# Kernel optimization log

Measured on AMD Instinct MI355X. Metric: run time of the kernel, lower is better.

Reference implementation:

```python
import jax, jax.numpy as jnp
import numpy as np

N_NODES = 50000
N_EDGES = 800000
D_IN = 128
D_HID = 128
BN_EPS = 1e-5


def _sage_mean(h, src, dst, w_self, w_neigh, b):
    # DGL SAGEConv('mean'): out = h @ W_self + mean_{neighbors}(h_src) @ W_neigh + bias
    msg = h[src]                                               # [E, D] gather
    ssum = jax.ops.segment_sum(msg, dst, num_segments=N_NODES)  # [N, D]
    deg = jax.ops.segment_sum(jnp.ones((src.shape[0],), h.dtype), dst,
                              num_segments=N_NODES)            # [N]
    mean = ssum / jnp.maximum(deg, 1.0)[:, None]
    return h @ w_self + mean @ w_neigh + b


def _bn_relu(h, gamma, beta):
    # BatchNorm1d with batch statistics (training-mode math), then ReLU.
    m = jnp.mean(h, axis=0)
    v = jnp.mean(jnp.square(h - m), axis=0)  # biased variance, as torch uses for normalization
    hn = (h - m) * jax.lax.rsqrt(v + BN_EPS) * gamma + beta
    return jax.nn.relu(hn)


def setup_inputs() -> dict:
    key = jax.random.key(0)
    ks = jax.random.split(key, 16)
    x = jax.random.normal(ks[0], (N_NODES, D_IN), dtype=jnp.float32)
    src = jax.random.randint(ks[1], (N_EDGES,), 0, N_NODES, dtype=jnp.int32)
    dst = jax.random.randint(ks[2], (N_EDGES,), 0, N_NODES, dtype=jnp.int32)
    s0 = 1.0 / np.sqrt(D_IN)
    s1 = 1.0 / np.sqrt(D_HID)
    inp = {
        'x': x, 'src': src, 'dst': dst,
        'W_self0': jax.random.uniform(ks[3], (D_IN, D_HID), jnp.float32, -s0, s0),
        'W_neigh0': jax.random.uniform(ks[4], (D_IN, D_HID), jnp.float32, -s0, s0),
        'b0': jnp.zeros((D_HID,), jnp.float32),
        'W_self1': jax.random.uniform(ks[5], (D_HID, D_HID), jnp.float32, -s1, s1),
        'W_neigh1': jax.random.uniform(ks[6], (D_HID, D_HID), jnp.float32, -s1, s1),
        'b1': jnp.zeros((D_HID,), jnp.float32),
        'W_self2': jax.random.uniform(ks[7], (D_HID, D_HID), jnp.float32, -s1, s1),
        'W_neigh2': jax.random.uniform(ks[8], (D_HID, D_HID), jnp.float32, -s1, s1),
        'b2': jnp.zeros((D_HID,), jnp.float32),
        'gamma0': jnp.ones((D_HID,), jnp.float32),
        'beta0': jnp.zeros((D_HID,), jnp.float32),
        'gamma1': jnp.ones((D_HID,), jnp.float32),
        'beta1': jnp.zeros((D_HID,), jnp.float32),
    }
    return inp


def reference(x, src, dst,
              W_self0, W_neigh0, b0,
              W_self1, W_neigh1, b1,
              W_self2, W_neigh2, b2,
              gamma0, beta0, gamma1, beta1):
    h = _sage_mean(x, src, dst, W_self0, W_neigh0, b0)
    h = _bn_relu(h, gamma0, beta0)  # dropout is identity in eval mode
    h = _sage_mean(h, src, dst, W_self1, W_neigh1, b1)
    h = _bn_relu(h, gamma1, beta1)
    h = _sage_mean(h, src, dst, W_self2, W_neigh2, b2)
    return h
```

## Files before the change

### kernel.cpp

```cpp
#include <hip/hip_runtime.h>

#define N_NODES 50000
#define N_EDGES 800000
#define D 128
#define BN_EPS 1e-5f

#define NBUCK 391
#define BSHIFT 7
#define S1_BLOCKS 256
#define EPB 3125
#define CVT_BLOCKS 6250
#define PACK_BLOCKS 384
#define NREP 16
#define NSLICE 16
#define SSHIFT 12
#define BN_BLOCKS 512

typedef __attribute__((ext_vector_type(8))) short bf16x8;
typedef __attribute__((ext_vector_type(4))) float f32x4;
typedef __attribute__((ext_vector_type(2))) float f32x2;

__device__ inline unsigned short f2bf(float f) {
    unsigned int u = __float_as_uint(f);
    u = (u + 0x7FFF + ((u >> 16) & 1)) >> 16;
    return (unsigned short)u;
}

__device__ inline float bf2f(unsigned short b) {
    return __uint_as_float(((unsigned)b) << 16);
}

__device__ __forceinline__ void acc_plain(f32x2* a, uint4 v) {
    unsigned w[4] = {v.x, v.y, v.z, v.w};
#pragma unroll
    for (int p = 0; p < 4; p++) {
        f32x2 f;
        f.x = __uint_as_float(w[p] << 16);
        f.y = __uint_as_float(w[p] & 0xffff0000u);
        a[p] += f;
    }
}


__global__ void fused_prep(const float* __restrict__ x, unsigned short* __restrict__ x16,
                           const int* __restrict__ dst, int* __restrict__ hist,
                           const float* __restrict__ Ws0, const float* __restrict__ Wn0,
                           const float* __restrict__ Ws1, const float* __restrict__ Wn1,
                           const float* __restrict__ Ws2, const float* __restrict__ Wn2,
                           unsigned short* __restrict__ Wf, float* __restrict__ statsg) {
    __shared__ int lh[NBUCK];
    const int bid = blockIdx.x, t = threadIdx.x;

    if (bid < CVT_BLOCKS) {
        int idx = bid * 256 + t;
        float4 v = ((const float4*)x)[idx];
        ushort4 o;
        o.x = f2bf(v.x); o.y = f2bf(v.y); o.z = f2bf(v.z); o.w = f2bf(v.w);
        ((ushort4*)x16)[idx] = o;
    } else if (bid < CVT_BLOCKS + S1_BLOCKS) {
        int blk = bid - CVT_BLOCKS;
        for (int i = t; i < NBUCK; i += 256) lh[i] = 0;
        __syncthreads();
        int e0 = blk * EPB;
        for (int i = 0; i < 13; i++) {
            int k = t + i * 256;
            if (k < EPB) atomicAdd(&lh[dst[e0 + k] >> BSHIFT], 1);
        }
        __syncthreads();
        for (int i = t; i < NBUCK; i += 256) hist[blk * NBUCK + i] = lh[i];
    } else {
        if (bid == CVT_BLOCKS + S1_BLOCKS) {
            for (int i = t; i < 2 * NREP * 256; i += 256) statsg[i] = 0.f;
        }
        int idx = (bid - (CVT_BLOCKS + S1_BLOCKS)) * 256 + t;
        if (idx < 3 * 32768) {
            int layer = idx >> 15;
            int rem = idx & 32767;
            int kt = rem >> 12;
            int nt = (rem >> 9) & 7;
            int lane = (rem >> 3) & 63;
            int j = rem & 7;
            int k = kt * 32 + (lane >> 4) * 8 + j;
            int n = nt * 16 + (lane & 15);
            const float* Wsrc;
            if (layer == 0) Wsrc = (k < 128) ? Ws0 : Wn0;
            else if (layer == 1) Wsrc = (k < 128) ? Ws1 : Wn1;
            else Wsrc = (k < 128) ? Ws2 : Wn2;
            Wf[idx] = f2bf(Wsrc[(k & 127) * D + n]);
        }
    }
}


__global__ void s2a(int* __restrict__ hist, int* __restrict__ bucketTotal) {
    __shared__ int s[S1_BLOCKS];
    int b = blockIdx.x, t = threadIdx.x;
    int v = hist[t * NBUCK + b];
    s[t] = v;
    __syncthreads();
    for (int off = 1; off < S1_BLOCKS; off <<= 1) {
        int x = (t >= off) ? s[t - off] : 0;
        __syncthreads();
        s[t] += x;
        __syncthreads();
    }
    hist[t * NBUCK + b] = s[t] - v;
    if (t == S1_BLOCKS - 1) bucketTotal[b] = s[t];
}


__global__ void s3_scatter(const int* __restrict__ src, const int* __restrict__ dst,
                           const int* __restrict__ hist, const int* __restrict__ bucketTotal,
                           int* __restrict__ bucketStart, unsigned int* __restrict__ rec) {
    __shared__ int sc[512];
    __shared__ int base[NBUCK];
    int blk = blockIdx.x, t = threadIdx.x;
    int i1 = t + 256;
    int v0 = (t < NBUCK) ? bucketTotal[t] : 0;
    int v1 = (i1 < NBUCK) ? bucketTotal[i1] : 0;
    sc[t] = v0; sc[i1] = v1;
    __syncthreads();
    for (int off = 1; off < 512; off <<= 1) {
        int x0 = (t >= off) ? sc[t - off] : 0;
        int x1 = (i1 >= off) ? sc[i1 - off] : 0;
        __syncthreads();
        sc[t] += x0; sc[i1] += x1;
        __syncthreads();
    }
    if (t < NBUCK)  base[t]  = (sc[t] - v0)  + hist[blk * NBUCK + t];
    if (i1 < NBUCK) base[i1] = (sc[i1] - v1) + hist[blk * NBUCK + i1];
    if (blk == 0) {
        if (t < NBUCK)  bucketStart[t]  = sc[t] - v0;
        if (i1 < NBUCK) bucketStart[i1] = sc[i1] - v1;
        if (t == 0) bucketStart[NBUCK] = N_EDGES;
    }
    __syncthreads();
    int e0 = blk * EPB;
    for (int i = 0; i < 13; i++) {
        int k = t + i * 256;
        if (k < EPB) {
            int e = e0 + k;
            int d = dst[e];
            int p = atomicAdd(&base[d >> BSHIFT], 1);
            rec[p] = ((unsigned)(d & 127) << 16) | (unsigned)src[e];
        }
    }
}


__global__ void s4_build(const unsigned int* __restrict__ rec, const int* __restrict__ bucketStart,
                         unsigned short* __restrict__ csr, int* __restrict__ degi,
                         int* __restrict__ offsets, float* __restrict__ inv_deg) {
    __shared__ int cnt[128 * NSLICE];
    __shared__ int exc[128 * NSLICE];
    __shared__ int lcur[128 * NSLICE];
    __shared__ int ls[256];
    int b = blockIdx.x, t = threadIdx.x;
    int start = bucketStart[b], end = bucketStart[b + 1];

    for (int i = t; i < 128 * NSLICE; i += 256) cnt[i] = 0;
    __syncthreads();
    for (int e = start + t; e < end; e += 256) {
        unsigned r = rec[e];
        int key = ((r >> 16) << 4) | ((r & 0xFFFFu) >> SSHIFT);
        atomicAdd(&cnt[key], 1);
    }
    __syncthreads();

    int cs[8];
    int sum8 = 0;
#pragma unroll
    for (int j = 0; j < 8; j++) { cs[j] = cnt[8 * t + j]; sum8 += cs[j]; }
    ls[t] = sum8;
    __syncthreads();
    for (int off = 1; off < 256; off <<= 1) {
        int x = (t >= off) ? ls[t - off] : 0;
        __syncthreads();
        ls[t] += x;
        __syncthreads();
    }
    int run = ls[t] - sum8;
#pragma unroll
    for (int j = 0; j < 8; j++) {
        exc[8 * t + j] = run;
        lcur[8 * t + j] = start + run;
        run += cs[j];
    }
    __syncthreads();

    if (t < 128) {
        int node = (b << BSHIFT) + t;
        int e0 = exc[t * NSLICE];
        int e1 = (t == 127) ? (end - start) : exc[(t + 1) * NSLICE];
        int v = e1 - e0;
        if (node < N_NODES) {
            degi[node] = v;
            offsets[node] = start + e0;
            inv_deg[node] = 1.0f / (float)max(v, 1);
        }
    }
    __syncthreads();
    for (int e = start + t; e < end; e += 256) {
        unsigned r = rec[e];
        int key = ((r >> 16) << 4) | ((r & 0xFFFFu) >> SSHIFT);
        int p = atomicAdd(&lcur[key], 1);
        csr[p] = (unsigned short)(r & 0xFFFFu);
    }
}


__global__ void bn_relu_apply(unsigned short* __restrict__ h,
                              const float* __restrict__ stats,
                              const float* __restrict__ gamma, const float* __restrict__ beta) {
    __shared__ float sc[128], sh[128];
    int t = threadIdx.x;
    if (t < 128) {
        const float invN = 1.0f / (float)N_NODES;
        float s = 0.f, q = 0.f;
#pragma unroll
        for (int r = 0; r < NREP; r++) {
            s += stats[r * 256 + t];
            q += stats[r * 256 + 128 + t];
        }
        float m = s * invN;
        float var = q * invN - m * m;
        float scv = rsqrtf(var + BN_EPS) * gamma[t];
        sc[t] = scv;
        sh[t] = beta[t] - m * scv;
    }
    __syncthreads();
    const int total = N_NODES * D / 8;
    for (int idx = blockIdx.x * 256 + t; idx < total; idx += BN_BLOCKS * 256) {
        uint4 v = ((const uint4*)h)[idx];
        int col0 = (idx & 15) * 8;
        unsigned w[4] = {v.x, v.y, v.z, v.w};
        unsigned ow[4];
#pragma unroll
        for (int p = 0; p < 4; p++) {
            float lo = __uint_as_float(w[p] << 16);
            float hi = __uint_as_float(w[p] & 0xffff0000u);
            float rlo = fmaxf(lo * sc[col0 + 2 * p]     + sh[col0 + 2 * p],     0.f);
            float rhi = fmaxf(hi * sc[col0 + 2 * p + 1] + sh[col0 + 2 * p + 1], 0.f);
            ow[p] = ((unsigned)f2bf(rhi) << 16) | f2bf(rlo);
        }
        uint4 o;
        o.x = ow[0]; o.y = ow[1]; o.z = ow[2]; o.w = ow[3];
        ((uint4*)h)[idx] = o;
    }
}


#define GROW(r) (*(const uint4*)(hb + ((size_t)(r) << 7)))
#define ROWIDX(k) __shfl((int)((k) < 16 ? cb0 : ((k) < 32 ? cb1 : cb2)), (k) & 15, 16)

__global__ void aggregate16(const unsigned short* __restrict__ h16,
                            const unsigned short* __restrict__ csr, const int* __restrict__ offsets,
                            const int* __restrict__ degi, const float* __restrict__ inv_deg,
                            unsigned short* __restrict__ mean16) {
    int t = threadIdx.x;
    int node = blockIdx.x * 16 + (t >> 4);
    int c = t & 15;
    const unsigned short* hb = h16 + c * 8;
    int beg = offsets[node], n = degi[node];

    int ci = beg + c;
    int cmax = N_EDGES - 1;
    unsigned cb0 = csr[min(ci, cmax)];
    unsigned cb1 = csr[min(ci + 16, cmax)];
    unsigned cb2 = csr[min(ci + 32, cmax)];

    f32x2 a[4];
#pragma unroll
    for (int j = 0; j < 4; j++) a[j] = (f32x2)(0.f);

    int nfast = n < 48 ? n : 48;
    int i = 0;
    if (nfast >= 4) {
        uint4 v0 = GROW(ROWIDX(0)), v1 = GROW(ROWIDX(1));
        uint4 v2 = GROW(ROWIDX(2)), v3 = GROW(ROWIDX(3));
        for (i = 4; i + 3 < nfast; i += 4) {
            int r0 = ROWIDX(i), r1 = ROWIDX(i + 1), r2 = ROWIDX(i + 2), r3 = ROWIDX(i + 3);
            uint4 w0 = GROW(r0), w1 = GROW(r1), w2 = GROW(r2), w3 = GROW(r3);
            acc_plain(a, v0); acc_plain(a, v1); acc_plain(a, v2); acc_plain(a, v3);
            v0 = w0; v1 = w1; v2 = w2; v3 = w3;
        }
        acc_plain(a, v0); acc_plain(a, v1); acc_plain(a, v2); acc_plain(a, v3);
    }
    for (; i < nfast; i++) { uint4 v = GROW(ROWIDX(i)); acc_plain(a, v); }
    for (; i < n; i++) { int r = csr[beg + i]; uint4 v = GROW(r); acc_plain(a, v); }

    float w = inv_deg[node];
    uint4 o;
    o.x = ((unsigned)f2bf(a[0].y * w) << 16) | f2bf(a[0].x * w);
    o.y = ((unsigned)f2bf(a[1].y * w) << 16) | f2bf(a[1].x * w);
    o.z = ((unsigned)f2bf(a[2].y * w) << 16) | f2bf(a[2].x * w);
    o.w = ((unsigned)f2bf(a[3].y * w) << 16) | f2bf(a[3].x * w);
    *(uint4*)(mean16 + (size_t)node * D + c * 8) = o;
}


__global__ __launch_bounds__(256, 4) void sage_gemm(
    const unsigned short* __restrict__ h16, const unsigned short* __restrict__ mean16,
    const unsigned short* __restrict__ Wf, const float* __restrict__ bias,
    unsigned short* __restrict__ out16, float* __restrict__ outf,
    float* __restrict__ statsOut) {
    __shared__ unsigned short sWf[16384];
    __shared__ float sstat[256];
    const int t = threadIdx.x;
    const int lane = t & 63;
    const int m = lane & 15;
    const int quad = lane >> 4;
    const int wrow0 = blockIdx.x * 64 + (t >> 6) * 16;

    int arow = wrow0 + m;
    if (arow >= N_NODES) arow = N_NODES - 1;

    bf16x8 afr[8];
#pragma unroll
    for (int kt = 0; kt < 4; kt++)
        afr[kt] = *(const bf16x8*)(h16 + (size_t)arow * D + kt * 32 + quad * 8);
#pragma unroll
    for (int kt = 0; kt < 4; kt++)
        afr[4 + kt] = *(const bf16x8*)(mean16 + (size_t)arow * D + kt * 32 + quad * 8);

    const uint4* W4 = (const uint4*)Wf;
    uint4* S4 = (uint4*)sWf;
#pragma unroll
    for (int i = 0; i < 8; i++) S4[i * 256 + t] = W4[i * 256 + t];
    if (statsOut) sstat[t] = 0.f;
    __syncthreads();

    f32x4 acc[8];
#pragma unroll
    for (int i = 0; i < 8; i++) acc[i] = (f32x4)(0.f);

#pragma unroll
    for (int kt = 0; kt < 4; kt++) {
#pragma unroll
        for (int nt = 0; nt < 8; nt++) {
            bf16x8 bf = *(const bf16x8*)(sWf + ((kt * 8 + nt) * 64 + lane) * 8);
            acc[nt] = __builtin_amdgcn_mfma_f32_16x16x32_bf16(afr[kt], bf, acc[nt], 0, 0, 0);
        }
    }

    __syncthreads();
#pragma unroll
    for (int i = 0; i < 8; i++) S4[i * 256 + t] = W4[2048 + i * 256 + t];
    __syncthreads();

#pragma unroll
    for (int kt = 4; kt < 8; kt++) {
#pragma unroll
        for (int nt = 0; nt < 8; nt++) {
            bf16x8 bf = *(const bf16x8*)(sWf + (((kt - 4) * 8 + nt) * 64 + lane) * 8);
            acc[nt] = __builtin_amdgcn_mfma_f32_16x16x32_bf16(afr[kt], bf, acc[nt], 0, 0, 0);
        }
    }

    const bool do16 = (out16 != nullptr);
#pragma unroll
    for (int nt = 0; nt < 8; nt++) {
        int cidx = nt * 16 + m;
        float bv = bias[cidx];
        float s = 0.f, q = 0.f;
#pragma unroll
        for (int reg = 0; reg < 4; reg++) {
            int r = wrow0 + quad * 4 + reg;
            float v = acc[nt][reg] + bv;
            if (r < N_NODES) {
                if (do16) out16[(size_t)r * D + cidx] = f2bf(v);
                else      outf[(size_t)r * D + cidx] = v;
                s += v; q += v * v;
            }
        }
        if (statsOut) {
            s += __shfl_xor(s, 16); s += __shfl_xor(s, 32);
            q += __shfl_xor(q, 16); q += __shfl_xor(q, 32);
            if (quad == 0) {
                atomicAdd(&sstat[cidx], s);
                atomicAdd(&sstat[128 + cidx], q);
            }
        }
    }
    if (statsOut) {
        __syncthreads();
        atomicAdd(&statsOut[(blockIdx.x & (NREP - 1)) * 256 + t], sstat[t]);
    }
}


extern "C" void kernel_launch(void* const* d_in, const int* in_sizes, int n_in,
                              void* d_out, int out_size, void* d_ws, size_t ws_size,
                              hipStream_t stream) {
    const float* x   = (const float*)d_in[0];
    const int* src   = (const int*)d_in[1];
    const int* dst   = (const int*)d_in[2];
    const float* Ws0 = (const float*)d_in[3];
    const float* Wn0 = (const float*)d_in[4];
    const float* b0  = (const float*)d_in[5];
    const float* Ws1 = (const float*)d_in[6];
    const float* Wn1 = (const float*)d_in[7];
    const float* b1  = (const float*)d_in[8];
    const float* Ws2 = (const float*)d_in[9];
    const float* Wn2 = (const float*)d_in[10];
    const float* b2  = (const float*)d_in[11];
    const float* g0  = (const float*)d_in[12];
    const float* be0 = (const float*)d_in[13];
    const float* g1  = (const float*)d_in[14];
    const float* be1 = (const float*)d_in[15];

    char* base = (char*)d_ws;
    size_t NND = (size_t)N_NODES * D;
    unsigned short* X16    = (unsigned short*)base;
    unsigned short* H16    = (unsigned short*)(base + NND * 2);
    unsigned short* mean16 = (unsigned short*)(base + 2 * NND * 2);
    char* p = base + 6 * NND;
    unsigned short* Wf = (unsigned short*)p;  p += 3 * 32768 * 2;
    int* hist          = (int*)p;             p += (size_t)S1_BLOCKS * NBUCK * 4;
    int* bucketTotal   = (int*)p;             p += 1568;
    int* bucketStart   = (int*)p;             p += 1600;
    unsigned int* rec  = (unsigned int*)p;    p += (size_t)N_EDGES * 4;
    unsigned short* csr = (unsigned short*)p; p += (size_t)N_EDGES * 2;
    int* degi    = (int*)p;                   p += N_NODES * 4;
    int* offsets = (int*)p;                   p += N_NODES * 4;
    float* inv_deg = (float*)p;               p += N_NODES * 4;
    float* stats   = (float*)p;               p += 2 * NREP * 256 * 4;
    float* stats0 = stats, *stats1 = stats + NREP * 256;

    fused_prep<<<CVT_BLOCKS + S1_BLOCKS + PACK_BLOCKS, 256, 0, stream>>>(
        x, X16, dst, hist, Ws0, Wn0, Ws1, Wn1, Ws2, Wn2, Wf, stats);
    s2a<<<NBUCK, 256, 0, stream>>>(hist, bucketTotal);
    s3_scatter<<<S1_BLOCKS, 256, 0, stream>>>(src, dst, hist, bucketTotal, bucketStart, rec);
    s4_build<<<NBUCK, 256, 0, stream>>>(rec, bucketStart, csr, degi, offsets, inv_deg);

    const int AGG_B = (N_NODES + 15) / 16;
    const int GEMM_B = (N_NODES + 63) / 64;

    aggregate16<<<AGG_B, 256, 0, stream>>>(X16, csr, offsets, degi, inv_deg, mean16);
    sage_gemm<<<GEMM_B, 256, 0, stream>>>(X16, mean16, Wf, b0, H16, nullptr, stats0);

    bn_relu_apply<<<BN_BLOCKS, 256, 0, stream>>>(H16, stats0, g0, be0);
    aggregate16<<<AGG_B, 256, 0, stream>>>(H16, csr, offsets, degi, inv_deg, mean16);
    sage_gemm<<<GEMM_B, 256, 0, stream>>>(H16, mean16, Wf + 32768, b1, X16, nullptr, stats1);

    bn_relu_apply<<<BN_BLOCKS, 256, 0, stream>>>(X16, stats1, g1, be1);
    aggregate16<<<AGG_B, 256, 0, stream>>>(X16, csr, offsets, degi, inv_deg, mean16);
    sage_gemm<<<GEMM_B, 256, 0, stream>>>(X16, mean16, Wf + 65536, b2, nullptr,
                                          (float*)d_out, nullptr);
}
```

Baseline: 278.8 us.

## Fuse BatchNorm+ReLU into consumer aggregation and GEMM kernels

Removes the standalone bn_relu_apply kernel, which made a full read-modify-write pass over the hidden features. Each consumer now applies normalization and ReLU itself: aggregate16 recomputes scale and shift from the stats and applies them to every gathered neighbor row, and sage_gemm applies them to its self-feature fragments before the MFMAs. This drops two launches and two passes over the feature matrix. The cost is extra per-edge FMA/max work in the gather loop and duplicated stat reductions in every block. NREP also drops from 16 to 4, which shrinks the per-block stat reduction but may add atomic contention on the stats.

```diff
diff --git a/kernel.cpp b/kernel.cpp
--- a/kernel.cpp
+++ b/kernel.cpp
@@ -11,10 +11,9 @@
 #define EPB 3125
 #define CVT_BLOCKS 6250
 #define PACK_BLOCKS 384
-#define NREP 16
+#define NREP 4
 #define NSLICE 16
 #define SSHIFT 12
-#define BN_BLOCKS 512
 
 typedef __attribute__((ext_vector_type(8))) short bf16x8;
 typedef __attribute__((ext_vector_type(4))) float f32x4;
@@ -38,6 +37,17 @@
         f.x = __uint_as_float(w[p] << 16);
         f.y = __uint_as_float(w[p] & 0xffff0000u);
         a[p] += f;
+    }
+}
+
+__device__ __forceinline__ void acc_bn(f32x2* a, uint4 v, const float* sc, const float* sh) {
+    unsigned w[4] = {v.x, v.y, v.z, v.w};
+#pragma unroll
+    for (int p = 0; p < 4; p++) {
+        float lo = __uint_as_float(w[p] << 16);
+        float hi = __uint_as_float(w[p] & 0xffff0000u);
+        a[p].x += fmaxf(lo * sc[2 * p]     + sh[2 * p],     0.f);
+        a[p].y += fmaxf(hi * sc[2 * p + 1] + sh[2 * p + 1], 0.f);
     }
 }
 
@@ -209,55 +219,35 @@
 }
 
 
-__global__ void bn_relu_apply(unsigned short* __restrict__ h,
-                              const float* __restrict__ stats,
-                              const float* __restrict__ gamma, const float* __restrict__ beta) {
-    __shared__ float sc[128], sh[128];
-    int t = threadIdx.x;
-    if (t < 128) {
-        const float invN = 1.0f / (float)N_NODES;
-        float s = 0.f, q = 0.f;
-#pragma unroll
-        for (int r = 0; r < NREP; r++) {
-            s += stats[r * 256 + t];
-            q += stats[r * 256 + 128 + t];
-        }
-        float m = s * invN;
-        float var = q * invN - m * m;
-        float scv = rsqrtf(var + BN_EPS) * gamma[t];
-        sc[t] = scv;
-        sh[t] = beta[t] - m * scv;
-    }
-    __syncthreads();
-    const int total = N_NODES * D / 8;
-    for (int idx = blockIdx.x * 256 + t; idx < total; idx += BN_BLOCKS * 256) {
-        uint4 v = ((const uint4*)h)[idx];
-        int col0 = (idx & 15) * 8;
-        unsigned w[4] = {v.x, v.y, v.z, v.w};
-        unsigned ow[4];
-#pragma unroll
-        for (int p = 0; p < 4; p++) {
-            float lo = __uint_as_float(w[p] << 16);
-            float hi = __uint_as_float(w[p] & 0xffff0000u);
-            float rlo = fmaxf(lo * sc[col0 + 2 * p]     + sh[col0 + 2 * p],     0.f);
-            float rhi = fmaxf(hi * sc[col0 + 2 * p + 1] + sh[col0 + 2 * p + 1], 0.f);
-            ow[p] = ((unsigned)f2bf(rhi) << 16) | f2bf(rlo);
-        }
-        uint4 o;
-        o.x = ow[0]; o.y = ow[1]; o.z = ow[2]; o.w = ow[3];
-        ((uint4*)h)[idx] = o;
-    }
-}
-
-
 #define GROW(r) (*(const uint4*)(hb + ((size_t)(r) << 7)))
 #define ROWIDX(k) __shfl((int)((k) < 16 ? cb0 : ((k) < 32 ? cb1 : cb2)), (k) & 15, 16)
 
 __global__ void aggregate16(const unsigned short* __restrict__ h16,
                             const unsigned short* __restrict__ csr, const int* __restrict__ offsets,
                             const int* __restrict__ degi, const float* __restrict__ inv_deg,
-                            unsigned short* __restrict__ mean16) {
+                            unsigned short* __restrict__ mean16,
+                            const float* __restrict__ statsIn,
+                            const float* __restrict__ gammaIn, const float* __restrict__ betaIn) {
+    __shared__ float lsc[128], lsh[128];
     int t = threadIdx.x;
+    if (statsIn) {
+        if (t < 128) {
+            const float invN = 1.0f / (float)N_NODES;
+            float s = 0.f, q = 0.f;
+#pragma unroll
+            for (int r = 0; r < NREP; r++) {
+                s += statsIn[r * 256 + t];
+                q += statsIn[r * 256 + 128 + t];
+            }
+            float m = s * invN;
+            float var = q * invN - m * m;
+            float scv = rsqrtf(var + BN_EPS) * gammaIn[t];
+            lsc[t] = scv;
+            lsh[t] = betaIn[t] - m * scv;
+        }
+        __syncthreads();
+    }
+
     int node = blockIdx.x * 16 + (t >> 4);
     int c = t & 15;
     const unsigned short* hb = h16 + c * 8;
@@ -275,19 +265,40 @@
 
     int nfast = n < 48 ? n : 48;
     int i = 0;
-    if (nfast >= 4) {
-        uint4 v0 = GROW(ROWIDX(0)), v1 = GROW(ROWIDX(1));
-        uint4 v2 = GROW(ROWIDX(2)), v3 = GROW(ROWIDX(3));
-        for (i = 4; i + 3 < nfast; i += 4) {
-            int r0 = ROWIDX(i), r1 = ROWIDX(i + 1), r2 = ROWIDX(i + 2), r3 = ROWIDX(i + 3);
-            uint4 w0 = GROW(r0), w1 = GROW(r1), w2 = GROW(r2), w3 = GROW(r3);
+    if (statsIn) {
+        float scv[8], shv[8];
+#pragma unroll
+        for (int j = 0; j < 8; j++) { scv[j] = lsc[c * 8 + j]; shv[j] = lsh[c * 8 + j]; }
+        if (nfast >= 4) {
+            uint4 v0 = GROW(ROWIDX(0)), v1 = GROW(ROWIDX(1));
+            uint4 v2 = GROW(ROWIDX(2)), v3 = GROW(ROWIDX(3));
+            for (i = 4; i + 3 < nfast; i += 4) {
+                int r0 = ROWIDX(i), r1 = ROWIDX(i + 1), r2 = ROWIDX(i + 2), r3 = ROWIDX(i + 3);
+                uint4 w0 = GROW(r0), w1 = GROW(r1), w2 = GROW(r2), w3 = GROW(r3);
+                acc_bn(a, v0, scv, shv); acc_bn(a, v1, scv, shv);
+                acc_bn(a, v2, scv, shv); acc_bn(a, v3, scv, shv);
+                v0 = w0; v1 = w1; v2 = w2; v3 = w3;
+            }
+            acc_bn(a, v0, scv, shv); acc_bn(a, v1, scv, shv);
+            acc_bn(a, v2, scv, shv); acc_bn(a, v3, scv, shv);
+        }
+        for (; i < nfast; i++) { uint4 v = GROW(ROWIDX(i)); acc_bn(a, v, scv, shv); }
+        for (; i < n; i++) { int r = csr[beg + i]; uint4 v = GROW(r); acc_bn(a, v, scv, shv); }
+    } else {
+        if (nfast >= 4) {
+            uint4 v0 = GROW(ROWIDX(0)), v1 = GROW(ROWIDX(1));
+            uint4 v2 = GROW(ROWIDX(2)), v3 = GROW(ROWIDX(3));
+            for (i = 4; i + 3 < nfast; i += 4) {
+                int r0 = ROWIDX(i), r1 = ROWIDX(i + 1), r2 = ROWIDX(i + 2), r3 = ROWIDX(i + 3);
+                uint4 w0 = GROW(r0), w1 = GROW(r1), w2 = GROW(r2), w3 = GROW(r3);
+                acc_plain(a, v0); acc_plain(a, v1); acc_plain(a, v2); acc_plain(a, v3);
+                v0 = w0; v1 = w1; v2 = w2; v3 = w3;
+            }
             acc_plain(a, v0); acc_plain(a, v1); acc_plain(a, v2); acc_plain(a, v3);
-            v0 = w0; v1 = w1; v2 = w2; v3 = w3;
-        }
-        acc_plain(a, v0); acc_plain(a, v1); acc_plain(a, v2); acc_plain(a, v3);
-    }
-    for (; i < nfast; i++) { uint4 v = GROW(ROWIDX(i)); acc_plain(a, v); }
-    for (; i < n; i++) { int r = csr[beg + i]; uint4 v = GROW(r); acc_plain(a, v); }
+        }
+        for (; i < nfast; i++) { uint4 v = GROW(ROWIDX(i)); acc_plain(a, v); }
+        for (; i < n; i++) { int r = csr[beg + i]; uint4 v = GROW(r); acc_plain(a, v); }
+    }
 
     float w = inv_deg[node];
     uint4 o;
@@ -303,9 +314,12 @@
     const unsigned short* __restrict__ h16, const unsigned short* __restrict__ mean16,
     const unsigned short* __restrict__ Wf, const float* __restrict__ bias,
     unsigned short* __restrict__ out16, float* __restrict__ outf,
-    float* __restrict__ statsOut) {
+    float* __restrict__ statsOut,
+    const float* __restrict__ statsIn,
+    const float* __restrict__ gammaIn, const float* __restrict__ betaIn) {
     __shared__ unsigned short sWf[16384];
     __shared__ float sstat[256];
+    __shared__ float lsc[128], lsh[128];
     const int t = threadIdx.x;
     const int lane = t & 63;
     const int m = lane & 15;
@@ -323,12 +337,39 @@
     for (int kt = 0; kt < 4; kt++)
         afr[4 + kt] = *(const bf16x8*)(mean16 + (size_t)arow * D + kt * 32 + quad * 8);
 
+    if (statsIn && t < 128) {
+        const float invN = 1.0f / (float)N_NODES;
+        float s = 0.f, q = 0.f;
+#pragma unroll
+        for (int r = 0; r < NREP; r++) {
+            s += statsIn[r * 256 + t];
+            q += statsIn[r * 256 + 128 + t];
+        }
+        float m2 = s * invN;
+        float var = q * invN - m2 * m2;
+        float scv = rsqrtf(var + BN_EPS) * gammaIn[t];
+        lsc[t] = scv;
+        lsh[t] = betaIn[t] - m2 * scv;
+    }
+
     const uint4* W4 = (const uint4*)Wf;
     uint4* S4 = (uint4*)sWf;
 #pragma unroll
     for (int i = 0; i < 8; i++) S4[i * 256 + t] = W4[i * 256 + t];
     if (statsOut) sstat[t] = 0.f;
     __syncthreads();
+
+    if (statsIn) {
+#pragma unroll
+        for (int kt = 0; kt < 4; kt++) {
+            int c0 = kt * 32 + quad * 8;
+#pragma unroll
+            for (int j = 0; j < 8; j++) {
+                float v = fmaxf(bf2f((unsigned short)afr[kt][j]) * lsc[c0 + j] + lsh[c0 + j], 0.f);
+                afr[kt][j] = (short)f2bf(v);
+            }
+        }
+    }
 
     f32x4 acc[8];
 #pragma unroll
@@ -436,15 +477,18 @@
     const int AGG_B = (N_NODES + 15) / 16;
     const int GEMM_B = (N_NODES + 63) / 64;
 
-    aggregate16<<<AGG_B, 256, 0, stream>>>(X16, csr, offsets, degi, inv_deg, mean16);
-    sage_gemm<<<GEMM_B, 256, 0, stream>>>(X16, mean16, Wf, b0, H16, nullptr, stats0);
-
-    bn_relu_apply<<<BN_BLOCKS, 256, 0, stream>>>(H16, stats0, g0, be0);
-    aggregate16<<<AGG_B, 256, 0, stream>>>(H16, csr, offsets, degi, inv_deg, mean16);
-    sage_gemm<<<GEMM_B, 256, 0, stream>>>(H16, mean16, Wf + 32768, b1, X16, nullptr, stats1);
-
-    bn_relu_apply<<<BN_BLOCKS, 256, 0, stream>>>(X16, stats1, g1, be1);
-    aggregate16<<<AGG_B, 256, 0, stream>>>(X16, csr, offsets, degi, inv_deg, mean16);
+    aggregate16<<<AGG_B, 256, 0, stream>>>(X16, csr, offsets, degi, inv_deg, mean16,
+                                           nullptr, nullptr, nullptr);
+    sage_gemm<<<GEMM_B, 256, 0, stream>>>(X16, mean16, Wf, b0, H16, nullptr,
+                                          stats0, nullptr, nullptr, nullptr);
+
+    aggregate16<<<AGG_B, 256, 0, stream>>>(H16, csr, offsets, degi, inv_deg, mean16,
+                                           stats0, g0, be0);
+    sage_gemm<<<GEMM_B, 256, 0, stream>>>(H16, mean16, Wf + 32768, b1, X16, nullptr,
+                                          stats1, stats0, g0, be0);
+
+    aggregate16<<<AGG_B, 256, 0, stream>>>(X16, csr, offsets, degi, inv_deg, mean16,
+                                           stats1, g1, be1);
     sage_gemm<<<GEMM_B, 256, 0, stream>>>(X16, mean16, Wf + 65536, b2, nullptr,
-                                          (float*)d_out, nullptr);
-}
+                                          (float*)d_out, nullptr, stats1, g1, be1);
+}
```

Measured after the change: 278.2 us, median of 2. About the same (-0.2%).
